# Performance work log

Hardware: AMD Instinct MI355X
Metric: run time of the kernel (lower is better)

Reference implementation:

```python
import jax, jax.numpy as jnp
import numpy as np

GAMMA = 0.9          # EMA momentum for prototype update
N_CLASSES = 201      # 200 classes + 1 background
K_PROTO = 5          # prototypes per class
FG_THRESH = 0.5      # pca_fg_threshold
SK_EPS = 0.05        # sinkhorn temperature (SwAV-style)
SK_ITERS = 3         # sinkhorn iterations
PCA_ITERS = 10       # niter of torch.pca_lowrank


def _l2norm(x, axis=-1):
    return x / jnp.maximum(jnp.linalg.norm(x, axis=axis, keepdims=True), 1e-12)


def _pca_first_component(X, key):
    # Randomized power iteration for the top left singular vector of the
    # centered data (mirrors torch.pca_lowrank(X, q=1, center=True, niter=10)).
    Xc = X - X.mean(0, keepdims=True)            # [N, D]
    G = Xc.T @ Xc                                # [D, D]
    v = jax.random.normal(key, (X.shape[1],), X.dtype)
    v = v / jnp.linalg.norm(v)
    def body(v, _):
        v = G @ v
        return v / jnp.maximum(jnp.linalg.norm(v), 1e-12), None
    v, _ = jax.lax.scan(body, v, None, length=PCA_ITERS)
    u = Xc @ v                                   # [N]
    return u / jnp.maximum(jnp.linalg.norm(u), 1e-12)


def _masked_sinkhorn(logits, mask):
    # logits: [C, BN, K], mask: [C, BN] bool (rows belonging to class c).
    # Vectorized equivalent of the per-class sinkhorn_knopp(L_c): returns a
    # row-stochastic assignment on the masked rows, balanced over the K cols.
    tiny = 1e-9
    m = mask[..., None].astype(logits.dtype)     # [C, BN, 1]
    Q = jnp.exp(logits / SK_EPS) * m
    n_c = jnp.maximum(mask.sum(-1).astype(logits.dtype), 1.0)[:, None, None]
    K = Q.shape[-1]
    Q = Q / jnp.maximum(Q.sum((-2, -1), keepdims=True), tiny)
    for _ in range(SK_ITERS):
        Q = Q / jnp.maximum(Q.sum(-2, keepdims=True), tiny) / K   # balance cols
        Q = Q * m
        Q = Q / jnp.maximum(Q.sum(-1, keepdims=True), tiny) / n_c # balance rows
        Q = Q * m
    return Q * n_c  # each masked row sums to 1


def setup_inputs() -> dict:
    key = jax.random.key(0)
    k1, k2, k3 = jax.random.split(key, 3)
    B, n_patches, dim = 32, 1024, 768
    patch_tokens = jax.random.normal(k1, (B, n_patches, dim), jnp.float32)
    prototypes = 0.02 * jax.random.normal(k2, (N_CLASSES, K_PROTO, dim), jnp.float32)
    labels = jax.random.randint(k3, (B,), 0, 200).astype(jnp.int64)
    return {"patch_tokens": patch_tokens, "prototypes": prototypes, "labels": labels}


def reference(patch_tokens, prototypes, labels):
    B, n_patches, D = patch_tokens.shape

    pt_norm = _l2norm(patch_tokens)              # [B, N, D]
    proto_norm = _l2norm(prototypes)             # [C, K, D]
    # B n_patches dim, C K dim -> B n_patches C K
    logits = jnp.einsum('bnd,ckd->bnck', pt_norm, proto_norm)

    # ---- get_pseudo_patch_labels (PCA foreground extraction) ----
    X = patch_tokens.reshape(-1, D)
    U = _pca_first_component(X, jax.random.key(1))
    U_scaled = (U - U.min()) / (U.max() - U.min())
    fg = (U_scaled < FG_THRESH).reshape(B, n_patches)
    patch_labels = jnp.where(fg, labels[:, None], N_CLASSES - 1)  # [B, N] int

    # ---- update_prototypes, vectorized over the 201-class python loop ----
    pl_flat = patch_labels.reshape(-1)                            # [B*N]
    L = jnp.transpose(logits.reshape(-1, N_CLASSES, K_PROTO), (1, 0, 2))  # [C, BN, K]
    class_ids = jnp.arange(N_CLASSES)
    mask = pl_flat[None, :] == class_ids[:, None]                 # [C, BN]
    Q = _masked_sinkhorn(L, mask)                                 # [C, BN, K]
    # P_c_new = L_c_assignment.T @ I_c, batched over classes
    P_new = jnp.einsum('cnk,nd->ckd', Q, pt_norm.reshape(-1, D))  # [C, K, D]
    present = (labels[None, :] == class_ids[:, None]).any(-1)     # 'c in labels'
    ema = GAMMA * prototypes + (1.0 - GAMMA) * P_new              # momentum_update
    new_prototypes = jnp.where(present[:, None, None], ema, prototypes)

    image_prototype_logits = logits.max(1)        # [B, C, K]
    class_logits = image_prototype_logits.sum(-1) # [B, C]
    return class_logits, image_prototype_logits, new_prototypes
```

## Files before the change

kernel.cpp:

```cpp
#include <hip/hip_runtime.h>
#include <stdint.h>
#include <stddef.h>

#define DEV static __device__ __forceinline__

typedef __attribute__((ext_vector_type(8))) short bf16x8;
typedef __attribute__((ext_vector_type(4))) float f32x4;

DEV float bf2f(unsigned short u){ union{unsigned int i; float f;} v; v.i = ((unsigned int)u)<<16; return v.f; }
DEV unsigned short f2bf(float f){ union{float f; unsigned int i;} v; v.f=f; unsigned int i=v.i;
  return (unsigned short)((i + 0x7FFFu + ((i>>16)&1u)) >> 16); }
DEV unsigned int fenc(float x){ unsigned int i = __float_as_uint(x); return (i & 0x80000000u) ? ~i : (i | 0x80000000u); }
DEV float fdec(unsigned int e){ unsigned int i = (e & 0x80000000u) ? (e & 0x7FFFFFFFu) : ~e; return __uint_as_float(i); }

DEV float waveSum(float s){
  for (int m=32;m;m>>=1) s += __shfl_xor(s, m, 64);
  return s;
}

DEV float blockSum(float v, float* red){
  int t = threadIdx.x;
  red[t] = v; __syncthreads();
  for (int k=128;k>0;k>>=1){ if (t<k) red[t] += red[t+k]; __syncthreads(); }
  float r = red[0]; __syncthreads();
  return r;
}

DEV void gl16(const unsigned short* g, unsigned short* lds){
  __builtin_amdgcn_global_load_lds(
      (const __attribute__((address_space(1))) void*)g,
      (__attribute__((address_space(3))) void*)lds, 16, 0, 0);
}

DEV float erfinv_f(float x){
  float w = -log1pf(-__fmul_rn(x,x));
  float p;
  if (w < 5.0f){
    w = w - 2.5f;
    p = 2.81022636e-08f;
    p = 3.43273939e-07f + p*w;
    p = -3.5233877e-06f + p*w;
    p = -4.39150654e-06f + p*w;
    p = 0.00021858087f + p*w;
    p = -0.00125372503f + p*w;
    p = -0.00417768164f + p*w;
    p = 0.246640727f + p*w;
    p = 1.50140941f + p*w;
  } else {
    w = sqrtf(w) - 3.0f;
    p = -0.000200214257f;
    p = 0.000100950558f + p*w;
    p = 0.00134934322f + p*w;
    p = -0.00367342844f + p*w;
    p = 0.00573950773f + p*w;
    p = -0.0076224613f + p*w;
    p = 0.00943887047f + p*w;
    p = 1.00167406f + p*w;
    p = 2.83297682f + p*w;
  }
  return p*x;
}

#define BN_TOT 32768
#define DIM 768
#define NCLS 201
#define KP 5
#define CKPAD 1024
#define GSPLIT 32
#define PSPLIT 8
#define LPAD 40


__global__ void k_setup(unsigned int* ipl_enc, int* cnt, int* cur, int* present,
                        unsigned int* minmax, float* meansum,
                        const int* __restrict__ raw, int* __restrict__ lab,
                        float* __restrict__ v){
  int i = blockIdx.x*256 + threadIdx.x;
  ipl_enc[i] = 0u;
  if (i < NCLS){ cnt[i]=0; cur[i]=0; present[i]=0; }
  if (i < DIM) meansum[i] = 0.f;
  if (i == 0){
    minmax[0]=0xFFFFFFFFu; minmax[1]=0u;
    bool is64 = true;
    for (int j=0;j<8;j++){
      int lo = raw[2*j], hi = raw[2*j+1];
      if (hi != 0 || lo < 0 || lo >= NCLS-1){ is64 = false; break; }
    }
    for (int j=0;j<32;j++) lab[j] = is64 ? raw[2*j] : raw[j];
  }
  if (i < DIM){
    unsigned int ks[3] = {0u, 1u, 0x1BD11BDBu};
    const int rot0[4] = {13,15,26,6};
    const int rot1[4] = {17,29,16,24};
    unsigned int x0 = 0u, x1 = (unsigned int)i;
    x0 += ks[0]; x1 += ks[1];
    #pragma unroll
    for (int g=0; g<5; g++){
      const int* rr = (g&1) ? rot1 : rot0;
      #pragma unroll
      for (int j=0;j<4;j++){
        x0 += x1;
        x1 = (x1 << rr[j]) | (x1 >> (32-rr[j]));
        x1 ^= x0;
      }
      x0 += ks[(g+1)%3];
      x1 += ks[(g+2)%3] + (unsigned int)(g+1);
    }
    unsigned int b = x0 ^ x1;
    const float lo = __uint_as_float(0xBF7FFFFFu);
    const float sq2 = __uint_as_float(0x3FB504F3u);
    float f = __uint_as_float((b>>9) | 0x3F800000u) - 1.0f;
    float uu = __fadd_rn(__fmul_rn(f, 2.0f), lo);
    uu = fmaxf(lo, uu);
    v[i] = sq2 * erfinv_f(uu);
  }
}

__global__ void k_proto(const float* __restrict__ protos, unsigned short* __restrict__ protn){
  int row = blockIdx.x;
  int l = threadIdx.x;
  if (row >= NCLS*KP){
    for (int j=0;j<12;j++) protn[(size_t)row*DIM + l + j*64] = 0;
    return;
  }
  const float* p = protos + (size_t)row*DIM;
  float x[12]; float s = 0.f;
  for (int j=0;j<12;j++){ x[j] = p[l + j*64]; s += x[j]*x[j]; }
  s = waveSum(s);
  float inv = 1.0f / fmaxf(sqrtf(s), 1e-12f);
  for (int j=0;j<12;j++) protn[(size_t)row*DIM + l + j*64] = f2bf(x[j]*inv);
}

__global__ void k_trans(const float* __restrict__ X, unsigned short* __restrict__ hiT,
                        unsigned short* __restrict__ loT, float* __restrict__ meansum){
  __shared__ float tile[64][65];
  __shared__ float colsum[4][64];
  int n0 = blockIdx.x*64, c0 = blockIdx.y*64;
  int t = threadIdx.x;
  float part = 0.f;
  for (int i=0;i<16;i++){
    int idx = t + i*256; int r = idx>>6, c = idx&63;
    float x = X[(size_t)(n0+r)*DIM + c0+c];
    tile[r][c] = x;
    part += x;
  }
  colsum[t>>6][t&63] = part;
  __syncthreads();
  for (int i=0;i<16;i++){
    int idx = t + i*256; int c = idx>>6, n = idx&63;
    float x = tile[n][c];
    unsigned short h = f2bf(x);
    float hf = bf2f(h);
    unsigned short lo = f2bf(x - hf);
    size_t o = (size_t)(c0+c)*BN_TOT + n0+n;
    hiT[o] = h; loT[o] = lo;
  }
  if (t < 64){
    float s = colsum[0][t]+colsum[1][t]+colsum[2][t]+colsum[3][t];
    atomicAdd(&meansum[c0+t], s);
  }
}

__global__ void k_ptn(const float* __restrict__ X, unsigned short* __restrict__ ptn){
  int row = blockIdx.x*4 + (threadIdx.x>>6);
  int l = threadIdx.x & 63;
  const float* p = X + (size_t)row*DIM;
  float x[12]; float s = 0.f;
  for (int j=0;j<12;j++){ x[j] = p[l + j*64]; s += x[j]*x[j]; }
  s = waveSum(s);
  float inv = 1.0f / fmaxf(sqrtf(s), 1e-12f);
  for (int j=0;j<12;j++) ptn[(size_t)row*DIM + l + j*64] = f2bf(x[j]*inv);
}

__global__ __launch_bounds__(256) void k_gemm_logits(const unsigned short* __restrict__ A,
                                                     const unsigned short* __restrict__ Bt,
                                                     unsigned int* __restrict__ ipl_enc){
  __shared__ __align__(16) unsigned short As[128][LPAD];
  __shared__ __align__(16) unsigned short Bs[128][LPAD];
  __shared__ float red[2][2][64];
  int flat = blockIdx.y*8 + blockIdx.x;
  int xcd = flat & 7, j = flat >> 3;
  int mb = xcd*32 + (j>>3);
  int nb = j & 7;
  int t = threadIdx.x;
  int w = t>>6, l = t&63;
  int wr = w>>1, wc = w&1;
  f32x4 acc[4][4];
  #pragma unroll
  for (int m=0;m<4;m++)
    #pragma unroll
    for (int n=0;n<4;n++){ acc[m][n][0]=0.f; acc[m][n][1]=0.f; acc[m][n][2]=0.f; acc[m][n][3]=0.f; }

  for (int kt=0; kt<24; kt++){
    int k0 = kt*32;
    __syncthreads();
    #pragma unroll
    for (int i=0;i<2;i++){
      int ch = t + i*256;
      int r = ch>>2, co = (ch&3)*8;
      *(uint4*)&As[r][co] = *(const uint4*)&A[(size_t)(mb*128 + r)*DIM + k0 + co];
      *(uint4*)&Bs[r][co] = *(const uint4*)&Bt[(size_t)(nb*128 + r)*DIM + k0 + co];
    }
    __syncthreads();
    bf16x8 a[4], b[4];
    #pragma unroll
    for (int m=0;m<4;m++) a[m] = *(const bf16x8*)&As[wr*64 + m*16 + (l&15)][(l>>4)*8];
    #pragma unroll
    for (int n=0;n<4;n++) b[n] = *(const bf16x8*)&Bs[wc*64 + n*16 + (l&15)][(l>>4)*8];
    #pragma unroll
    for (int m=0;m<4;m++)
      #pragma unroll
      for (int n=0;n<4;n++)
        acc[m][n] = __builtin_amdgcn_mfma_f32_16x16x32_bf16(a[m], b[n], acc[m][n], 0,0,0);
  }
  float vmax[4];
  #pragma unroll
  for (int n=0;n<4;n++){
    float v = -1e30f;
    #pragma unroll
    for (int m=0;m<4;m++)
      #pragma unroll
      for (int r=0;r<4;r++) v = fmaxf(v, acc[m][n][r]);
    v = fmaxf(v, __shfl_xor(v, 16, 64));
    v = fmaxf(v, __shfl_xor(v, 32, 64));
    vmax[n] = v;
  }
  __syncthreads();
  if (l < 16){
    #pragma unroll
    for (int n=0;n<4;n++) red[wc][wr][n*16 + l] = vmax[n];
  }
  __syncthreads();
  if (t < 128){
    int wcc = t>>6, col = t&63;
    float v = fmaxf(red[wcc][0][col], red[wcc][1][col]);
    int gcol = nb*128 + wcc*64 + col;
    if (gcol < NCLS*KP){
      int b = (mb*128) >> 10;
      atomicMax(&ipl_enc[b*CKPAD + gcol], fenc(v));
    }
  }
}

__global__ __launch_bounds__(256) void k_gemm_G(const unsigned short* __restrict__ hiT,
                                                const unsigned short* __restrict__ loT,
                                                float* __restrict__ Gpart){
  __shared__ __align__(16) unsigned short Ahi[128*32];
  __shared__ __align__(16) unsigned short Alo[128*32];
  __shared__ __align__(16) unsigned short Bhi[128*32];
  __shared__ __align__(16) unsigned short Blo[128*32];
  int b = blockIdx.x;
  int xcd = b & 7, q = b >> 3;
  int s = xcd + 8*(q/21);
  int p = q % 21;
  int ib = 0, rem = p;
  while (rem >= 6 - ib){ rem -= 6 - ib; ib++; }
  int jb = ib + rem;
  int t = threadIdx.x, w = t>>6, l = t&63;
  int wr = w>>1, wc = w&1;

  int gu = (l&3) ^ ((l>>2)&3) ^ (l>>4);
  size_t lane_off = (size_t)(l>>2)*BN_TOT + (size_t)gu*8;
  size_t baseA = (size_t)(ib*128)*BN_TOT;
  size_t baseB = (size_t)(jb*128)*BN_TOT;

  int physc = (l>>4) ^ (l&3) ^ ((l>>2)&3);
  int rdA = (wr*64 + (l&15))*32 + physc*8;
  int rdB = (wc*64 + (l&15))*32 + physc*8;

  f32x4 acc[4][4];
  #pragma unroll
  for (int m=0;m<4;m++)
    #pragma unroll
    for (int n=0;n<4;n++){ acc[m][n][0]=0.f; acc[m][n][1]=0.f; acc[m][n][2]=0.f; acc[m][n][3]=0.f; }

  for (int kt=0; kt<32; kt++){
    size_t k0 = (size_t)s*1024 + (size_t)kt*32;
    __syncthreads();
    #pragma unroll
    for (int ci=0; ci<2; ci++){
      int c = w + ci*4;
      size_t roff = (size_t)(c*16)*BN_TOT + k0 + lane_off;
      gl16(hiT + baseA + roff, &Ahi[c*512]);
      gl16(loT + baseA + roff, &Alo[c*512]);
      gl16(hiT + baseB + roff, &Bhi[c*512]);
      gl16(loT + baseB + roff, &Blo[c*512]);
    }
    __syncthreads();
    bf16x8 bh[4], bl[4];
    #pragma unroll
    for (int n=0;n<4;n++){
      bh[n] = *(const bf16x8*)&Bhi[rdB + n*512];
      bl[n] = *(const bf16x8*)&Blo[rdB + n*512];
    }
    #pragma unroll
    for (int m=0;m<4;m++){
      bf16x8 ah = *(const bf16x8*)&Ahi[rdA + m*512];
      bf16x8 al = *(const bf16x8*)&Alo[rdA + m*512];
      #pragma unroll
      for (int n=0;n<4;n++){
        acc[m][n] = __builtin_amdgcn_mfma_f32_16x16x32_bf16(ah, bh[n], acc[m][n], 0,0,0);
        acc[m][n] = __builtin_amdgcn_mfma_f32_16x16x32_bf16(ah, bl[n], acc[m][n], 0,0,0);
        acc[m][n] = __builtin_amdgcn_mfma_f32_16x16x32_bf16(al, bh[n], acc[m][n], 0,0,0);
      }
    }
  }

  float* out = Gpart + (size_t)s*DIM*DIM;
  #pragma unroll
  for (int m=0;m<4;m++)
    #pragma unroll
    for (int n=0;n<4;n++)
      #pragma unroll
      for (int r=0;r<4;r++){
        int row = ib*128 + wr*64 + m*16 + (l>>4)*4 + r;
        int col = jb*128 + wc*64 + n*16 + (l&15);
        out[(size_t)row*DIM + col] = acc[m][n][r];
        if (ib != jb) out[(size_t)col*DIM + row] = acc[m][n][r];
      }
}

__global__ void k_gfix(const float* __restrict__ Gpart, const float* __restrict__ meansum,
                       float* __restrict__ G){
  int i = blockIdx.x*256 + threadIdx.x;
  int r = i/DIM, c = i%DIM;
  float s = 0.f;
  for (int p=0;p<GSPLIT;p++) s += Gpart[(size_t)p*DIM*DIM + i];
  const float invN = 1.0f/32768.0f;
  float mr = meansum[r]*invN, mc = meansum[c]*invN;
  G[i] = s*invN - mr*mc;
}

__global__ void k_mv(const float* __restrict__ G, const float* __restrict__ vin,
                     float* __restrict__ vout){
  __shared__ float vs[DIM];
  int t = threadIdx.x;
  for (int i=t;i<DIM;i+=256) vs[i] = vin[i];
  __syncthreads();
  int row = blockIdx.x*4 + (t>>6), l = t&63;
  const float* g = G + (size_t)row*DIM;
  float s = 0.f;
  for (int j=0;j<12;j++) s += g[l + j*64]*vs[l + j*64];
  s = waveSum(s);
  if (l==0) vout[row] = s;
}

__global__ void k_muv(const float* __restrict__ meansum, const float* __restrict__ v,
                      float* __restrict__ scal){
  __shared__ float red[256];
  int t = threadIdx.x;
  float s = 0.f;
  for (int i=t;i<DIM;i+=256) s += meansum[i]*(1.0f/32768.0f)*v[i];
  float r = blockSum(s, red);
  if (t==0) scal[0] = r;
}

__global__ void k_u(const float* __restrict__ X, const float* __restrict__ v,
                    const float* __restrict__ scal,
                    float* __restrict__ u, unsigned int* __restrict__ minmax){
  __shared__ float vs[DIM];
  __shared__ float smn[4], smx[4];
  int t = threadIdx.x;
  for (int i=t;i<DIM;i+=256) vs[i] = v[i];
  __syncthreads();
  int w = t>>6, l = t&63;
  float mn = 1e30f, mx = -1e30f;
  #pragma unroll
  for (int rr=0; rr<4; rr++){
    int row = blockIdx.x*16 + w*4 + rr;
    const float4* xr = (const float4*)(X + (size_t)row*DIM);
    float s = 0.f;
    #pragma unroll
    for (int j=0;j<3;j++){
      float4 x4 = xr[l + j*64];
      int base = 4*(l + j*64);
      s += x4.x*vs[base] + x4.y*vs[base+1] + x4.z*vs[base+2] + x4.w*vs[base+3];
    }
    s = waveSum(s);
    if (l==0){
      float val = s - scal[0];
      u[row] = val;
      mn = fminf(mn, val); mx = fmaxf(mx, val);
    }
  }
  if (l==0){ smn[w]=mn; smx[w]=mx; }
  __syncthreads();
  if (t==0){
    for (int k=1;k<4;k++){ mn = fminf(mn, smn[k]); mx = fmaxf(mx, smx[k]); }
    atomicMin(&minmax[0], fenc(mn));
    atomicMax(&minmax[1], fenc(mx));
  }
}

__global__ void k_pl(const float* __restrict__ u, const int* __restrict__ labels,
                     const unsigned int* __restrict__ minmax, int* __restrict__ pl,
                     int* __restrict__ cnt){
  int n = blockIdx.x*256 + threadIdx.x;
  float umin = fdec(minmax[0]), umax = fdec(minmax[1]);
  float us = (u[n]-umin)/(umax-umin);
  int c = (us < 0.5f) ? labels[n>>10] : (NCLS-1);
  pl[n] = c;
  if (c < NCLS-1) atomicAdd(&cnt[c], 1);
}

__global__ void k_offs(const int* __restrict__ cnt, int* __restrict__ offs,
                       const int* __restrict__ labels, int* __restrict__ present){
  if (threadIdx.x == 0){
    int acc = 0;
    for (int c=0;c<NCLS-1;c++){ offs[c] = acc; acc += cnt[c]; }
    offs[NCLS-1] = acc;
  }
  if (threadIdx.x < 32) atomicOr(&present[labels[threadIdx.x]], 1);
}

__global__ void k_scatter(const int* __restrict__ pl, const int* __restrict__ offs,
                          int* __restrict__ cur, int* __restrict__ idx){
  int n = blockIdx.x*256 + threadIdx.x;
  int c = pl[n];
  if (c < NCLS-1){
    int p = offs[c] + atomicAdd(&cur[c], 1);
    idx[p] = n;
  }
}

__global__ void k_qlog(const int* __restrict__ idx, const int* __restrict__ offs,
                       const int* __restrict__ pl, const unsigned short* __restrict__ ptn,
                       const unsigned short* __restrict__ protn, float* __restrict__ q){
  int i = blockIdx.x*4 + (threadIdx.x>>6);
  int l = threadIdx.x & 63;
  int total = offs[NCLS-1];
  if (i >= total) return;
  int n = idx[i];
  int c = pl[n];
  const unsigned short* pr = ptn + (size_t)n*DIM;
  float x[12];
  for (int j=0;j<12;j++) x[j] = bf2f(pr[l + j*64]);
  for (int k=0;k<KP;k++){
    const unsigned short* wv = protn + (size_t)(c*KP + k)*DIM;
    float s = 0.f;
    for (int j=0;j<12;j++) s += x[j]*bf2f(wv[l + j*64]);
    s = waveSum(s);
    if (l==0) q[(size_t)i*KP + k] = expf(s*20.0f);
  }
}

__global__ void k_sink(const int* __restrict__ cnt, const int* __restrict__ offs,
                       float* __restrict__ q){
  __shared__ float red[256];
  __shared__ float colf[KP];
  int c = blockIdx.x;
  int nc = cnt[c];
  if (nc == 0) return;
  int n0 = offs[c];
  float* Q = q + (size_t)n0*KP;
  int t = threadIdx.x;
  int tot5 = nc*KP;
  float s = 0.f;
  for (int i=t;i<tot5;i+=256) s += Q[i];
  float total = blockSum(s, red);
  float sc = 1.0f/fmaxf(total, 1e-9f);
  for (int i=t;i<tot5;i+=256) Q[i] *= sc;
  __syncthreads();
  float ncf = (float)nc;
  for (int it=0; it<3; it++){
    float cs[KP] = {0,0,0,0,0};
    for (int i=t;i<nc;i+=256){
      const float* row = Q + (size_t)i*KP;
      #pragma unroll
      for (int k=0;k<KP;k++) cs[k] += row[k];
    }
    for (int k=0;k<KP;k++){
      float v = blockSum(cs[k], red);
      if (t==0) colf[k] = 1.0f/(fmaxf(v,1e-9f)*(float)KP);
    }
    __syncthreads();
    for (int i=t;i<nc;i+=256){
      float* row = Q + (size_t)i*KP;
      float qq[KP]; float rs = 0.f;
      #pragma unroll
      for (int k=0;k<KP;k++){ qq[k] = row[k]*colf[k]; rs += qq[k]; }
      float rf = 1.0f/(fmaxf(rs,1e-9f)*ncf);
      #pragma unroll
      for (int k=0;k<KP;k++) row[k] = qq[k]*rf;
    }
    __syncthreads();
  }
  for (int i=t;i<tot5;i+=256) Q[i] *= ncf;
}

__global__ void k_pnew(const int* __restrict__ cnt, const int* __restrict__ offs,
                       const int* __restrict__ present, const int* __restrict__ idx,
                       const float* __restrict__ q, const unsigned short* __restrict__ ptn,
                       float* __restrict__ P4){
  int c = blockIdx.y, s = blockIdx.x;
  if (!present[c]) return;
  int nc = cnt[c], n0 = offs[c];
  int r0 = n0 + (nc*s)/PSPLIT;
  int r1 = n0 + (nc*(s+1))/PSPLIT;
  int t = threadIdx.x;
  float acc[KP][3];
  #pragma unroll
  for (int k=0;k<KP;k++){ acc[k][0]=0.f; acc[k][1]=0.f; acc[k][2]=0.f; }
  for (int i=r0; i<r1; ++i){
    int n = idx[i];
    float qv[KP];
    #pragma unroll
    for (int k=0;k<KP;k++) qv[k] = q[(size_t)i*KP + k];
    const unsigned short* row = ptn + (size_t)n*DIM;
    #pragma unroll
    for (int j=0;j<3;j++){
      float x = bf2f(row[t + j*256]);
      #pragma unroll
      for (int k=0;k<KP;k++) acc[k][j] += qv[k]*x;
    }
  }
  float* out = P4 + ((size_t)(s*NCLS + c)*KP)*DIM;
  #pragma unroll
  for (int k=0;k<KP;k++)
    #pragma unroll
    for (int j=0;j<3;j++)
      out[(size_t)k*DIM + t + j*256] = acc[k][j];
}

__global__ void k_ema(const float* __restrict__ protos, const float* __restrict__ P4,
                      const int* __restrict__ present, float* __restrict__ out){
  int i = blockIdx.x*256 + threadIdx.x;
  if (i >= NCLS*KP*DIM) return;
  int c = i / (KP*DIM);
  float p = protos[i];
  if (present[c]){
    float s = 0.f;
    #pragma unroll
    for (int sp=0; sp<PSPLIT; sp++) s += P4[(size_t)sp*NCLS*KP*DIM + i];
    out[i] = 0.9f*p + 0.1f*s;
  } else {
    out[i] = p;
  }
}

__global__ void k_final(const unsigned int* __restrict__ ipl_enc, float* __restrict__ out){
  int i = blockIdx.x*256 + threadIdx.x;
  if (i < 32*NCLS*KP){
    int b = i / (NCLS*KP), ck = i % (NCLS*KP);
    out[32*NCLS + i] = fdec(ipl_enc[b*CKPAD + ck]);
  }
  if (i < 32*NCLS){
    int b = i / NCLS, c = i % NCLS;
    float s = 0.f;
    #pragma unroll
    for (int k=0;k<KP;k++) s += fdec(ipl_enc[b*CKPAD + c*KP + k]);
    out[b*NCLS + c] = s;
  }
}

extern "C" void kernel_launch(void* const* d_in, const int* in_sizes, int n_in,
                              void* d_out, int out_size, void* d_ws, size_t ws_size,
                              hipStream_t stream){
  (void)in_sizes; (void)n_in; (void)out_size; (void)ws_size;
  const float* X = (const float*)d_in[0];
  const float* protos = (const float*)d_in[1];
  const int* labels_raw = (const int*)d_in[2];
  float* out = (float*)d_out;

  char* w = (char*)d_ws;
  size_t off = 0;
  auto alloc = [&](size_t bytes)->void*{
    void* p = (void*)(w + off);
    off = (off + bytes + 255) & ~(size_t)255;
    return p;
  };
  unsigned short* hiT   = (unsigned short*)alloc((size_t)DIM*BN_TOT*2);
  unsigned short* loT   = (unsigned short*)alloc((size_t)DIM*BN_TOT*2);
  unsigned short* ptn   = (unsigned short*)alloc((size_t)BN_TOT*DIM*2);
  unsigned short* protn = (unsigned short*)alloc((size_t)CKPAD*DIM*2);
  float* Gpart   = (float*)alloc((size_t)GSPLIT*DIM*DIM*4);
  float* G       = (float*)alloc((size_t)DIM*DIM*4);
  float* meansum = (float*)alloc(DIM*4);
  float* vA      = (float*)alloc(DIM*4);
  float* vB      = (float*)alloc(DIM*4);
  float* scal    = (float*)alloc(256);
  int* cnt       = (int*)alloc(1024);
  int* cur       = (int*)alloc(1024);
  int* offs      = (int*)alloc(1024);
  int* present   = (int*)alloc(1024);
  int* labc      = (int*)alloc(256);
  unsigned int* minmax  = (unsigned int*)alloc(256);
  unsigned int* ipl_enc = (unsigned int*)alloc((size_t)32*CKPAD*4);

  char* gb = (char*)Gpart;
  size_t goff = 0;
  auto galloc = [&](size_t bytes)->void*{
    void* p = (void*)(gb + goff);
    goff = (goff + bytes + 255) & ~(size_t)255;
    return p;
  };
  float* u_  = (float*)galloc(BN_TOT*4);
  int* pl_   = (int*)galloc(BN_TOT*4);
  int* idx_  = (int*)galloc(BN_TOT*4);
  float* q_  = (float*)galloc((size_t)BN_TOT*KP*4);
  float* P4_ = (float*)galloc((size_t)PSPLIT*NCLS*KP*DIM*4);

  dim3 b256(256);
  k_setup<<<dim3(128), b256, 0, stream>>>(ipl_enc, cnt, cur, present, minmax, meansum,
                                          labels_raw, labc, vA);
  k_proto<<<dim3(CKPAD), dim3(64), 0, stream>>>(protos, protn);
  k_trans<<<dim3(512,12), b256, 0, stream>>>(X, hiT, loT, meansum);
  k_ptn<<<dim3(8192), b256, 0, stream>>>(X, ptn);
  k_gemm_logits<<<dim3(8,256), b256, 0, stream>>>(ptn, protn, ipl_enc);
  k_gemm_G<<<dim3(21*GSPLIT), b256, 0, stream>>>(hiT, loT, Gpart);
  k_gfix<<<dim3(2304), b256, 0, stream>>>(Gpart, meansum, G);
  for (int it=0; it<10; it++){
    float* src = (it&1) ? vB : vA;
    float* dst = (it&1) ? vA : vB;
    k_mv<<<dim3(192), b256, 0, stream>>>(G, src, dst);
  }
  k_muv<<<dim3(1), b256, 0, stream>>>(meansum, vA, scal);
  k_u<<<dim3(2048), b256, 0, stream>>>(X, vA, scal, u_, minmax);
  k_pl<<<dim3(128), b256, 0, stream>>>(u_, labc, minmax, pl_, cnt);
  k_offs<<<dim3(1), b256, 0, stream>>>(cnt, offs, labc, present);
  k_scatter<<<dim3(128), b256, 0, stream>>>(pl_, offs, cur, idx_);
  k_qlog<<<dim3(8192), b256, 0, stream>>>(idx_, offs, pl_, ptn, protn, q_);
  k_sink<<<dim3(200), b256, 0, stream>>>(cnt, offs, q_);
  k_pnew<<<dim3(PSPLIT,NCLS), b256, 0, stream>>>(cnt, offs, present, idx_, q_, ptn, P4_);
  k_ema<<<dim3(3015), b256, 0, stream>>>(protos, P4_, present, out + 32*NCLS + 32*NCLS*KP);
  k_final<<<dim3(126), b256, 0, stream>>>(ipl_enc, out);
}
```

Baseline: 509.8 us.

## Fuse power iterations into one kernel, swizzle logits GEMM loads, widen G split

The ten separate matrix-vector launches and the mean-projection launch are replaced by one persistent 64-block kernel. Each block keeps its 12 rows of G in shared memory, and the blocks synchronise through an atomic grid barrier between iterations. The logits GEMM now uses direct global-to-LDS loads with an XOR-swizzled layout in place of register-staged padded tiles. The G GEMM k-split grows to 64 when the workspace allows it, which raises parallelism but also adds more partial sums for the fix-up kernel to reduce. The grid barrier assumes all 64 blocks are co-resident and that the barrier counter is reset every call.

```diff
diff --git a/kernel.cpp b/kernel.cpp
--- a/kernel.cpp
+++ b/kernel.cpp
@@ -30,6 +30,17 @@
   __builtin_amdgcn_global_load_lds(
       (const __attribute__((address_space(1))) void*)g,
       (__attribute__((address_space(3))) void*)lds, 16, 0, 0);
+}
+
+DEV void gbar(unsigned int* bar, unsigned int target){
+  __syncthreads();
+  if (threadIdx.x==0){
+    __threadfence();
+    atomicAdd(bar, 1u);
+    while (atomicAdd(bar, 0u) < target) __builtin_amdgcn_s_sleep(2);
+    __threadfence();
+  }
+  __syncthreads();
 }
 
 DEV float erfinv_f(float x){
@@ -66,19 +77,18 @@
 #define NCLS 201
 #define KP 5
 #define CKPAD 1024
-#define GSPLIT 32
 #define PSPLIT 8
-#define LPAD 40
 
 
 __global__ void k_setup(unsigned int* ipl_enc, int* cnt, int* cur, int* present,
                         unsigned int* minmax, float* meansum,
                         const int* __restrict__ raw, int* __restrict__ lab,
-                        float* __restrict__ v){
+                        float* __restrict__ v, unsigned int* bar){
   int i = blockIdx.x*256 + threadIdx.x;
   ipl_enc[i] = 0u;
   if (i < NCLS){ cnt[i]=0; cur[i]=0; present[i]=0; }
   if (i < DIM) meansum[i] = 0.f;
+  if (i < 8) bar[i] = 0u;
   if (i == 0){
     minmax[0]=0xFFFFFFFFu; minmax[1]=0u;
     bool is64 = true;
@@ -175,8 +185,8 @@
 __global__ __launch_bounds__(256) void k_gemm_logits(const unsigned short* __restrict__ A,
                                                      const unsigned short* __restrict__ Bt,
                                                      unsigned int* __restrict__ ipl_enc){
-  __shared__ __align__(16) unsigned short As[128][LPAD];
-  __shared__ __align__(16) unsigned short Bs[128][LPAD];
+  __shared__ __align__(16) unsigned short As[128*32];
+  __shared__ __align__(16) unsigned short Bs[128*32];
   __shared__ float red[2][2][64];
   int flat = blockIdx.y*8 + blockIdx.x;
   int xcd = flat & 7, j = flat >> 3;
@@ -185,6 +195,16 @@
   int t = threadIdx.x;
   int w = t>>6, l = t&63;
   int wr = w>>1, wc = w&1;
+
+  int gu = (l&3) ^ ((l>>2)&3) ^ (l>>4);
+  size_t lane_off = (size_t)(l>>2)*DIM + (size_t)gu*8;
+  size_t baseA = (size_t)(mb*128)*DIM;
+  size_t baseB = (size_t)(nb*128)*DIM;
+
+  int physc = (l>>4) ^ (l&3) ^ ((l>>2)&3);
+  int rdA = (wr*64 + (l&15))*32 + physc*8;
+  int rdB = (wc*64 + (l&15))*32 + physc*8;
+
   f32x4 acc[4][4];
   #pragma unroll
   for (int m=0;m<4;m++)
@@ -192,21 +212,21 @@
     for (int n=0;n<4;n++){ acc[m][n][0]=0.f; acc[m][n][1]=0.f; acc[m][n][2]=0.f; acc[m][n][3]=0.f; }
 
   for (int kt=0; kt<24; kt++){
-    int k0 = kt*32;
+    size_t k0 = (size_t)kt*32;
     __syncthreads();
     #pragma unroll
-    for (int i=0;i<2;i++){
-      int ch = t + i*256;
-      int r = ch>>2, co = (ch&3)*8;
-      *(uint4*)&As[r][co] = *(const uint4*)&A[(size_t)(mb*128 + r)*DIM + k0 + co];
-      *(uint4*)&Bs[r][co] = *(const uint4*)&Bt[(size_t)(nb*128 + r)*DIM + k0 + co];
+    for (int ci=0; ci<2; ci++){
+      int c = w + ci*4;
+      size_t roff = (size_t)(c*16)*DIM + k0 + lane_off;
+      gl16(A + baseA + roff, &As[c*512]);
+      gl16(Bt + baseB + roff, &Bs[c*512]);
     }
     __syncthreads();
     bf16x8 a[4], b[4];
     #pragma unroll
-    for (int m=0;m<4;m++) a[m] = *(const bf16x8*)&As[wr*64 + m*16 + (l&15)][(l>>4)*8];
-    #pragma unroll
-    for (int n=0;n<4;n++) b[n] = *(const bf16x8*)&Bs[wc*64 + n*16 + (l&15)][(l>>4)*8];
+    for (int m=0;m<4;m++) a[m] = *(const bf16x8*)&As[rdA + m*512];
+    #pragma unroll
+    for (int n=0;n<4;n++) b[n] = *(const bf16x8*)&Bs[rdB + n*512];
     #pragma unroll
     for (int m=0;m<4;m++)
       #pragma unroll
@@ -244,7 +264,8 @@
 
 __global__ __launch_bounds__(256) void k_gemm_G(const unsigned short* __restrict__ hiT,
                                                 const unsigned short* __restrict__ loT,
-                                                float* __restrict__ Gpart){
+                                                float* __restrict__ Gpart,
+                                                int kspan, int ktiters){
   __shared__ __align__(16) unsigned short Ahi[128*32];
   __shared__ __align__(16) unsigned short Alo[128*32];
   __shared__ __align__(16) unsigned short Bhi[128*32];
@@ -274,8 +295,8 @@
     #pragma unroll
     for (int n=0;n<4;n++){ acc[m][n][0]=0.f; acc[m][n][1]=0.f; acc[m][n][2]=0.f; acc[m][n][3]=0.f; }
 
-  for (int kt=0; kt<32; kt++){
-    size_t k0 = (size_t)s*1024 + (size_t)kt*32;
+  for (int kt=0; kt<ktiters; kt++){
+    size_t k0 = (size_t)s*kspan + (size_t)kt*32;
     __syncthreads();
     #pragma unroll
     for (int ci=0; ci<2; ci++){
@@ -321,38 +342,49 @@
 }
 
 __global__ void k_gfix(const float* __restrict__ Gpart, const float* __restrict__ meansum,
-                       float* __restrict__ G){
+                       float* __restrict__ G, int nsplit){
   int i = blockIdx.x*256 + threadIdx.x;
   int r = i/DIM, c = i%DIM;
   float s = 0.f;
-  for (int p=0;p<GSPLIT;p++) s += Gpart[(size_t)p*DIM*DIM + i];
+  for (int p=0;p<nsplit;p++) s += Gpart[(size_t)p*DIM*DIM + i];
   const float invN = 1.0f/32768.0f;
   float mr = meansum[r]*invN, mc = meansum[c]*invN;
   G[i] = s*invN - mr*mc;
 }
 
-__global__ void k_mv(const float* __restrict__ G, const float* __restrict__ vin,
-                     float* __restrict__ vout){
+__global__ __launch_bounds__(256) void k_power(const float* __restrict__ G,
+                                               float* __restrict__ vA, float* __restrict__ vB,
+                                               const float* __restrict__ meansum,
+                                               float* __restrict__ scal,
+                                               unsigned int* __restrict__ bar){
+  __shared__ float gl[12][DIM];
   __shared__ float vs[DIM];
-  int t = threadIdx.x;
-  for (int i=t;i<DIM;i+=256) vs[i] = vin[i];
-  __syncthreads();
-  int row = blockIdx.x*4 + (t>>6), l = t&63;
-  const float* g = G + (size_t)row*DIM;
-  float s = 0.f;
-  for (int j=0;j<12;j++) s += g[l + j*64]*vs[l + j*64];
-  s = waveSum(s);
-  if (l==0) vout[row] = s;
-}
-
-__global__ void k_muv(const float* __restrict__ meansum, const float* __restrict__ v,
-                      float* __restrict__ scal){
   __shared__ float red[256];
-  int t = threadIdx.x;
-  float s = 0.f;
-  for (int i=t;i<DIM;i+=256) s += meansum[i]*(1.0f/32768.0f)*v[i];
-  float r = blockSum(s, red);
-  if (t==0) scal[0] = r;
+  int t = threadIdx.x, b = blockIdx.x;
+  for (int i=t; i<12*DIM; i+=256) gl[i/DIM][i%DIM] = G[(size_t)b*12*DIM + i];
+  int wv = t>>6, l = t&63;
+  for (int it=0; it<10; it++){
+    const float* src = (it&1) ? vB : vA;
+    float* dst = (it&1) ? vA : vB;
+    for (int i=t;i<DIM;i+=256) vs[i] = src[i];
+    __syncthreads();
+    #pragma unroll
+    for (int rr=0; rr<3; rr++){
+      int row = wv*3 + rr;
+      float s = 0.f;
+      #pragma unroll
+      for (int j=0;j<12;j++) s += gl[row][l + j*64]*vs[l + j*64];
+      s = waveSum(s);
+      if (l==0) dst[b*12 + row] = s;
+    }
+    gbar(bar, 64u*(unsigned)(it+1));
+  }
+  if (b == 0){
+    float s = 0.f;
+    for (int i=t;i<DIM;i+=256) s += meansum[i]*(1.0f/32768.0f)*vA[i];
+    float r = blockSum(s, red);
+    if (t==0) scal[0] = r;
+  }
 }
 
 __global__ void k_u(const float* __restrict__ X, const float* __restrict__ v,
@@ -556,7 +588,7 @@
 extern "C" void kernel_launch(void* const* d_in, const int* in_sizes, int n_in,
                               void* d_out, int out_size, void* d_ws, size_t ws_size,
                               hipStream_t stream){
-  (void)in_sizes; (void)n_in; (void)out_size; (void)ws_size;
+  (void)in_sizes; (void)n_in; (void)out_size;
   const float* X = (const float*)d_in[0];
   const float* protos = (const float*)d_in[1];
   const int* labels_raw = (const int*)d_in[2];
@@ -573,7 +605,6 @@
   unsigned short* loT   = (unsigned short*)alloc((size_t)DIM*BN_TOT*2);
   unsigned short* ptn   = (unsigned short*)alloc((size_t)BN_TOT*DIM*2);
   unsigned short* protn = (unsigned short*)alloc((size_t)CKPAD*DIM*2);
-  float* Gpart   = (float*)alloc((size_t)GSPLIT*DIM*DIM*4);
   float* G       = (float*)alloc((size_t)DIM*DIM*4);
   float* meansum = (float*)alloc(DIM*4);
   float* vA      = (float*)alloc(DIM*4);
@@ -584,8 +615,15 @@
   int* offs      = (int*)alloc(1024);
   int* present   = (int*)alloc(1024);
   int* labc      = (int*)alloc(256);
+  unsigned int* bar     = (unsigned int*)alloc(256);
   unsigned int* minmax  = (unsigned int*)alloc(256);
   unsigned int* ipl_enc = (unsigned int*)alloc((size_t)32*CKPAD*4);
+
+  size_t per = (size_t)DIM*DIM*4;
+  int nsplit = (off + 64*per <= ws_size) ? 64 : 32;
+  float* Gpart = (float*)alloc((size_t)nsplit*per);
+  int kspan = BN_TOT / nsplit;
+  int ktiters = kspan / 32;
 
   char* gb = (char*)Gpart;
   size_t goff = 0;
@@ -602,19 +640,14 @@
 
   dim3 b256(256);
   k_setup<<<dim3(128), b256, 0, stream>>>(ipl_enc, cnt, cur, present, minmax, meansum,
-                                          labels_raw, labc, vA);
+                                          labels_raw, labc, vA, bar);
   k_proto<<<dim3(CKPAD), dim3(64), 0, stream>>>(protos, protn);
   k_trans<<<dim3(512,12), b256, 0, stream>>>(X, hiT, loT, meansum);
   k_ptn<<<dim3(8192), b256, 0, stream>>>(X, ptn);
   k_gemm_logits<<<dim3(8,256), b256, 0, stream>>>(ptn, protn, ipl_enc);
-  k_gemm_G<<<dim3(21*GSPLIT), b256, 0, stream>>>(hiT, loT, Gpart);
-  k_gfix<<<dim3(2304), b256, 0, stream>>>(Gpart, meansum, G);
-  for (int it=0; it<10; it++){
-    float* src = (it&1) ? vB : vA;
-    float* dst = (it&1) ? vA : vB;
-    k_mv<<<dim3(192), b256, 0, stream>>>(G, src, dst);
-  }
-  k_muv<<<dim3(1), b256, 0, stream>>>(meansum, vA, scal);
+  k_gemm_G<<<dim3(21*nsplit), b256, 0, stream>>>(hiT, loT, Gpart, kspan, ktiters);
+  k_gfix<<<dim3(2304), b256, 0, stream>>>(Gpart, meansum, G, nsplit);
+  k_power<<<dim3(64), b256, 0, stream>>>(G, vA, vB, meansum, scal, bar);
   k_u<<<dim3(2048), b256, 0, stream>>>(X, vA, scal, u_, minmax);
   k_pl<<<dim3(128), b256, 0, stream>>>(u_, labc, minmax, pl_, cnt);
   k_offs<<<dim3(1), b256, 0, stream>>>(cnt, offs, labc, present);
```

New measurement: 589.0 us. 15.5% more time.

## Vectorize ptn, use direct-to-LDS swizzled loads in logits GEMM, fold k_muv into k_u

Applied to the files above, without the earlier changes.

The normalization kernel now loads float4 and stores packed bf16x4 instead of scalar accesses. The logits GEMM drops the padded LDS tiles and loads 16-byte chunks straight into a swizzled LDS layout through a gl16 helper, with matching XOR-swizzled read offsets so bank conflicts stay low without padding. The single-block k_muv launch is removed and every k_u block recomputes the mean·v scalar itself, which saves one launch but repeats a small reduction in 2048 blocks.

```diff
diff --git a/kernel.cpp b/kernel.cpp
--- a/kernel.cpp
+++ b/kernel.cpp
@@ -68,7 +68,6 @@
 #define CKPAD 1024
 #define GSPLIT 32
 #define PSPLIT 8
-#define LPAD 40
 
 
 __global__ void k_setup(unsigned int* ipl_enc, int* cnt, int* cur, int* present,
@@ -164,19 +163,29 @@
 __global__ void k_ptn(const float* __restrict__ X, unsigned short* __restrict__ ptn){
   int row = blockIdx.x*4 + (threadIdx.x>>6);
   int l = threadIdx.x & 63;
-  const float* p = X + (size_t)row*DIM;
-  float x[12]; float s = 0.f;
-  for (int j=0;j<12;j++){ x[j] = p[l + j*64]; s += x[j]*x[j]; }
+  const float4* xr = (const float4*)(X + (size_t)row*DIM);
+  float4 x4[3]; float s = 0.f;
+  #pragma unroll
+  for (int j=0;j<3;j++){
+    x4[j] = xr[l + j*64];
+    s += x4[j].x*x4[j].x + x4[j].y*x4[j].y + x4[j].z*x4[j].z + x4[j].w*x4[j].w;
+  }
   s = waveSum(s);
   float inv = 1.0f / fmaxf(sqrtf(s), 1e-12f);
-  for (int j=0;j<12;j++) ptn[(size_t)row*DIM + l + j*64] = f2bf(x[j]*inv);
+  #pragma unroll
+  for (int j=0;j<3;j++){
+    ushort4 o;
+    o.x = f2bf(x4[j].x*inv); o.y = f2bf(x4[j].y*inv);
+    o.z = f2bf(x4[j].z*inv); o.w = f2bf(x4[j].w*inv);
+    *(ushort4*)&ptn[(size_t)row*DIM + 4*(l + j*64)] = o;
+  }
 }
 
 __global__ __launch_bounds__(256) void k_gemm_logits(const unsigned short* __restrict__ A,
                                                      const unsigned short* __restrict__ Bt,
                                                      unsigned int* __restrict__ ipl_enc){
-  __shared__ __align__(16) unsigned short As[128][LPAD];
-  __shared__ __align__(16) unsigned short Bs[128][LPAD];
+  __shared__ __align__(16) unsigned short As[128*32];
+  __shared__ __align__(16) unsigned short Bs[128*32];
   __shared__ float red[2][2][64];
   int flat = blockIdx.y*8 + blockIdx.x;
   int xcd = flat & 7, j = flat >> 3;
@@ -185,6 +194,16 @@
   int t = threadIdx.x;
   int w = t>>6, l = t&63;
   int wr = w>>1, wc = w&1;
+
+  int gu = (l&3) ^ ((l>>2)&3) ^ (l>>4);
+  size_t lane_off = (size_t)(l>>2)*DIM + (size_t)gu*8;
+  size_t baseA = (size_t)(mb*128)*DIM;
+  size_t baseB = (size_t)(nb*128)*DIM;
+
+  int physc = (l>>4) ^ (l&3) ^ ((l>>2)&3);
+  int rdA = (wr*64 + (l&15))*32 + physc*8;
+  int rdB = (wc*64 + (l&15))*32 + physc*8;
+
   f32x4 acc[4][4];
   #pragma unroll
   for (int m=0;m<4;m++)
@@ -192,21 +211,21 @@
     for (int n=0;n<4;n++){ acc[m][n][0]=0.f; acc[m][n][1]=0.f; acc[m][n][2]=0.f; acc[m][n][3]=0.f; }
 
   for (int kt=0; kt<24; kt++){
-    int k0 = kt*32;
+    size_t k0 = (size_t)kt*32;
     __syncthreads();
     #pragma unroll
-    for (int i=0;i<2;i++){
-      int ch = t + i*256;
-      int r = ch>>2, co = (ch&3)*8;
-      *(uint4*)&As[r][co] = *(const uint4*)&A[(size_t)(mb*128 + r)*DIM + k0 + co];
-      *(uint4*)&Bs[r][co] = *(const uint4*)&Bt[(size_t)(nb*128 + r)*DIM + k0 + co];
+    for (int ci=0; ci<2; ci++){
+      int c = w + ci*4;
+      size_t roff = (size_t)(c*16)*DIM + k0 + lane_off;
+      gl16(A + baseA + roff, &As[c*512]);
+      gl16(Bt + baseB + roff, &Bs[c*512]);
     }
     __syncthreads();
     bf16x8 a[4], b[4];
     #pragma unroll
-    for (int m=0;m<4;m++) a[m] = *(const bf16x8*)&As[wr*64 + m*16 + (l&15)][(l>>4)*8];
-    #pragma unroll
-    for (int n=0;n<4;n++) b[n] = *(const bf16x8*)&Bs[wc*64 + n*16 + (l&15)][(l>>4)*8];
+    for (int m=0;m<4;m++) a[m] = *(const bf16x8*)&As[rdA + m*512];
+    #pragma unroll
+    for (int n=0;n<4;n++) b[n] = *(const bf16x8*)&Bs[rdB + n*512];
     #pragma unroll
     for (int m=0;m<4;m++)
       #pragma unroll
@@ -345,24 +364,18 @@
   if (l==0) vout[row] = s;
 }
 
-__global__ void k_muv(const float* __restrict__ meansum, const float* __restrict__ v,
-                      float* __restrict__ scal){
-  __shared__ float red[256];
-  int t = threadIdx.x;
-  float s = 0.f;
-  for (int i=t;i<DIM;i+=256) s += meansum[i]*(1.0f/32768.0f)*v[i];
-  float r = blockSum(s, red);
-  if (t==0) scal[0] = r;
-}
-
 __global__ void k_u(const float* __restrict__ X, const float* __restrict__ v,
-                    const float* __restrict__ scal,
+                    const float* __restrict__ meansum,
                     float* __restrict__ u, unsigned int* __restrict__ minmax){
   __shared__ float vs[DIM];
+  __shared__ float red[256];
   __shared__ float smn[4], smx[4];
   int t = threadIdx.x;
   for (int i=t;i<DIM;i+=256) vs[i] = v[i];
   __syncthreads();
+  float ps = 0.f;
+  for (int i=t;i<DIM;i+=256) ps += meansum[i]*(1.0f/32768.0f)*vs[i];
+  float scal = blockSum(ps, red);
   int w = t>>6, l = t&63;
   float mn = 1e30f, mx = -1e30f;
   #pragma unroll
@@ -378,7 +391,7 @@
     }
     s = waveSum(s);
     if (l==0){
-      float val = s - scal[0];
+      float val = s - scal;
       u[row] = val;
       mn = fminf(mn, val); mx = fmaxf(mx, val);
     }
@@ -578,7 +591,6 @@
   float* meansum = (float*)alloc(DIM*4);
   float* vA      = (float*)alloc(DIM*4);
   float* vB      = (float*)alloc(DIM*4);
-  float* scal    = (float*)alloc(256);
   int* cnt       = (int*)alloc(1024);
   int* cur       = (int*)alloc(1024);
   int* offs      = (int*)alloc(1024);
@@ -614,8 +626,7 @@
     float* dst = (it&1) ? vA : vB;
     k_mv<<<dim3(192), b256, 0, stream>>>(G, src, dst);
   }
-  k_muv<<<dim3(1), b256, 0, stream>>>(meansum, vA, scal);
-  k_u<<<dim3(2048), b256, 0, stream>>>(X, vA, scal, u_, minmax);
+  k_u<<<dim3(2048), b256, 0, stream>>>(X, vA, meansum, u_, minmax);
   k_pl<<<dim3(128), b256, 0, stream>>>(u_, labc, minmax, pl_, cnt);
   k_offs<<<dim3(1), b256, 0, stream>>>(cnt, offs, labc, present);
   k_scatter<<<dim3(128), b256, 0, stream>>>(pl_, offs, cur, idx_);
```

Result: no change. 502.1 us (-1.5%).
